# Optimization experiments

Hardware: AMD Instinct MI355X
Metric: run time of the kernel (lower is better)

The kernel has to match this reference:

```python
import jax, jax.numpy as jnp
import numpy as np

EPS = 1e-12  # F.normalize default eps


def _unfold(x, k, pad, stride):
    # torch F.unfold: [B,C,H,W] -> [B, C*k*k, L], features ordered (c, kh, kw), L row-major.
    B, C, H, W = x.shape
    xp = jnp.pad(x, ((0, 0), (0, 0), (pad, pad), (pad, pad)))
    Ho = (H + 2 * pad - k) // stride + 1
    Wo = (W + 2 * pad - k) // stride + 1
    r = (jnp.arange(Ho) * stride)[:, None] + jnp.arange(k)[None, :]  # [Ho,k]
    c = (jnp.arange(Wo) * stride)[:, None] + jnp.arange(k)[None, :]  # [Wo,k]
    p = xp[:, :, r[:, None, :, None], c[None, :, None, :]]  # [B,C,Ho,Wo,k,k]
    return p.transpose(0, 1, 4, 5, 2, 3).reshape(B, C * k * k, Ho * Wo)


def _fold(p, out_hw, k, pad, stride):
    # torch F.fold: overlap-add inverse of _unfold.
    B, CKK, L = p.shape
    C = CKK // (k * k)
    H, W = out_hw
    Ho = (H + 2 * pad - k) // stride + 1
    Wo = (W + 2 * pad - k) // stride + 1
    p = p.reshape(B, C, k, k, Ho, Wo).transpose(0, 1, 4, 5, 2, 3)  # [B,C,Ho,Wo,k,k]
    r = (jnp.arange(Ho) * stride)[:, None] + jnp.arange(k)[None, :]
    c = (jnp.arange(Wo) * stride)[:, None] + jnp.arange(k)[None, :]
    out = jnp.zeros((B, C, H + 2 * pad, W + 2 * pad), p.dtype)
    out = out.at[:, :, r[:, None, :, None], c[None, :, None, :]].add(p)
    return out[:, :, pad:pad + H, pad:pad + W]


def _l2n(x, axis):
    n = jnp.sqrt(jnp.sum(x * x, axis=axis, keepdims=True))
    return x / jnp.maximum(n, EPS)


def setup_inputs() -> dict:
    key = jax.random.key(0)
    ks = jax.random.split(key, 11)
    B, H, W = 1, 32, 32
    f = jnp.float32
    return {
        'lrsr_lv3': jax.random.normal(ks[0], (B, 256, H, W), f),
        'refsr_lv1': jax.random.normal(ks[1], (B, 64, 4 * H, 4 * W), f),
        'refsr_lv2': jax.random.normal(ks[2], (B, 128, 2 * H, 2 * W), f),
        'refsr_lv3': jax.random.normal(ks[3], (B, 256, H, W), f),
        'ref_lv1': jax.random.normal(ks[4], (B, 64, 4 * H, 4 * W), f),
        'ref_lv2': jax.random.normal(ks[5], (B, 128, 2 * H, 2 * W), f),
        'ref_lv3': jax.random.normal(ks[6], (B, 256, H, W), f),
        'W1': jax.random.normal(ks[7], (2304, 1152), f) * 0.02,
        'b1': jax.random.normal(ks[8], (2304,), f) * 0.02,
        'W2': jax.random.normal(ks[9], (2304, 576), f) * 0.02,
        'b2': jax.random.normal(ks[10], (2304,), f) * 0.02,
    }


def reference(lrsr_lv3, refsr_lv1, refsr_lv2, refsr_lv3, ref_lv1, ref_lv2, ref_lv3, W1, b1, W2, b2):
    B, _, H, W = lrsr_lv3.shape
    lr3 = _unfold(lrsr_lv3, 3, 1, 1)                       # [B, 2304, N]
    r3 = _unfold(refsr_lv3, 3, 1, 1).transpose(0, 2, 1)    # [B, N3, 2304]
    r2 = _unfold(refsr_lv2, 3, 1, 1).transpose(0, 2, 1) @ W1.T + b1  # [B, N2, 2304]
    r1 = _unfold(refsr_lv1, 3, 1, 1).transpose(0, 2, 1) @ W2.T + b2  # [B, N1, 2304]
    r3 = _l2n(r3, 2); r2 = _l2n(r2, 2); r1 = _l2n(r1, 2)
    lr3 = _l2n(lr3, 1)
    R3 = jnp.einsum('bnd,bdm->bnm', r3, lr3)  # [B, N3, N]
    R2 = jnp.einsum('bnd,bdm->bnm', r2, lr3)  # [B, N2, N]
    R1 = jnp.einsum('bnd,bdm->bnm', r1, lr3)  # [B, N1, N]
    R3_star = jnp.max(R3, axis=1); R3_arg = jnp.argmax(R3, axis=1)
    R2_star = jnp.max(R2, axis=1)
    R1_star = jnp.max(R1, axis=1)
    ref3u = _unfold(ref_lv3, 3, 1, 1)
    ref2u = _unfold(ref_lv2, 6, 2, 2)
    ref1u = _unfold(ref_lv1, 12, 4, 4)
    idx = R3_arg[:, None, :]  # [B,1,N] broadcast over feature dim
    T3u = jnp.take_along_axis(ref3u, idx, axis=2)
    T2u = jnp.take_along_axis(ref2u, idx, axis=2)
    T1u = jnp.take_along_axis(ref1u, idx, axis=2)
    T_lv3 = _fold(T3u, (H, W), 3, 1, 1) / 9.0
    T_lv2 = _fold(T2u, (2 * H, 2 * W), 6, 2, 2) / 9.0
    T_lv1 = _fold(T1u, (4 * H, 4 * W), 12, 4, 4) / 9.0
    S_3 = R3_star.reshape(B, 1, H, W)
    S_2 = R2_star.reshape(B, 1, H, W)
    S_1 = R1_star.reshape(B, 1, H, W)
    return (S_1, S_2, S_3, T_lv3, T_lv2, T_lv1)
```

## Files before the change

### kernel.cpp

```cpp
#include <hip/hip_runtime.h>

typedef short bf8 __attribute__((ext_vector_type(8)));
typedef float f32x4 __attribute__((ext_vector_type(4)));

static __device__ __forceinline__ unsigned short f2bf(float f) {
  unsigned u = __float_as_uint(f);
  unsigned r = u + 0x7FFFu + ((u >> 16) & 1u);
  return (unsigned short)(r >> 16);
}
static __device__ __forceinline__ float bf2f(unsigned short h) {
  return __uint_as_float(((unsigned)h) << 16);
}
static __device__ __forceinline__ unsigned fkey(float f) {
  unsigned u = __float_as_uint(f);
  return (u & 0x80000000u) ? ~u : (u | 0x80000000u);
}
static __device__ __forceinline__ float kdec(unsigned k) {
  unsigned u = (k & 0x80000000u) ? (k & 0x7FFFFFFFu) : ~k;
  return __uint_as_float(u);
}
static __device__ __forceinline__ int xcdswz(int h, int nwg) {
  int q = nwg >> 3, r = nwg & 7;
  int xcd = h & 7, w = h >> 3;
  return (xcd < r ? xcd * (q + 1) : r * (q + 1) + (xcd - r) * q) + w;
}
static __device__ __forceinline__ int xcdbal(int h, int nwg, int nb0) {
  int xcd = h & 7, w = h >> 3;
  int qa = nb0 >> 3, qb = (nwg - nb0) >> 3;
  return (w < qa) ? (xcd * qa + w) : (nb0 + xcd * qb + (w - qa));
}
static __device__ __forceinline__ float win9s(const float* __restrict__ b, int m) {
  int mi = m >> 5, mj = m & 31;
  float s = 0.f;
#pragma unroll
  for (int dy = -1; dy <= 1; ++dy) {
    int i = mi + dy; if ((unsigned)i >= 32u) continue;
#pragma unroll
    for (int dx = -1; dx <= 1; ++dx) {
      int jx = mj + dx; if ((unsigned)jx >= 32u) continue;
      s += b[i * 32 + jx];
    }
  }
  return s;
}

static __device__ __forceinline__ void gload_lds16(const unsigned short* g, unsigned short* l) {
  __builtin_amdgcn_global_load_lds((const __attribute__((address_space(1))) void*)g,
                                   (__attribute__((address_space(3))) void*)l, 16, 0, 0);
}

static __device__ __forceinline__ float uf3(const float* __restrict__ src, int lgS, int d, int m) {
  const int S = 1 << lgS;
  int cc = d / 9;
  int r9 = d - cc * 9;
  int ki = r9 / 3;
  int kj = r9 - ki * 3;
  int i = (m >> lgS) + ki - 1;
  int j = (m & (S - 1)) + kj - 1;
  if ((unsigned)i >= (unsigned)S || (unsigned)j >= (unsigned)S) return 0.f;
  return src[((size_t)cc << (2 * lgS)) + ((size_t)i << lgS) + j];
}

__global__ __launch_bounds__(256) void k_prepA(const float* __restrict__ lrsr3, const float* __restrict__ rsr3,
                                               const float* __restrict__ rsr2, const float* __restrict__ rsr1,
                                               const float* __restrict__ W1, const float* __restrict__ W2,
                                               const float* __restrict__ b1, const float* __restrict__ b2,
                                               float* __restrict__ G2,
                                               float* __restrict__ rsr2t, float* __restrict__ rsr1t,
                                               unsigned short* __restrict__ lr3nbT,
                                               unsigned short* __restrict__ W1t, unsigned short* __restrict__ W2t,
                                               float* __restrict__ sclw, float* __restrict__ scu3w,
                                               float* __restrict__ D1, float* __restrict__ D2) {
  __shared__ __align__(16) unsigned char smem[18432];
  const int blk = blockIdx.x;
  const int tid = threadIdx.x;
  if (blk < 4) {
    float* b1L = (float*)smem;
    float* b2L = b1L + 2304;
    const int p = blk * 256 + tid;
    for (int i = tid; i < 2304; i += 256) { b1L[i] = b1[i]; b2L[i] = b2[i]; }
    __syncthreads();
    float d1a[9] = {}, d2a[9] = {};
    for (int cc = 0; cc < 256; ++cc) {
      float v = lrsr3[(size_t)cc * 1024 + p];
#pragma unroll
      for (int kk = 0; kk < 9; ++kk) {
        d1a[kk] = fmaf(b1L[cc * 9 + kk], v, d1a[kk]);
        d2a[kk] = fmaf(b2L[cc * 9 + kk], v, d2a[kk]);
      }
    }
#pragma unroll
    for (int kk = 0; kk < 9; ++kk) { D1[kk * 1024 + p] = d1a[kk]; D2[kk * 1024 + p] = d2a[kk]; }
  } else if (blk < 6) {
    float* ss = (float*)smem;
    const float* src = (blk == 4) ? lrsr3 : rsr3;
    float a4[4] = {0.f, 0.f, 0.f, 0.f};
    for (int cc = 0; cc < 256; ++cc) {
#pragma unroll
      for (int k = 0; k < 4; ++k) {
        float v = src[(size_t)cc * 1024 + k * 256 + tid];
        a4[k] = fmaf(v, v, a4[k]);
      }
    }
#pragma unroll
    for (int k = 0; k < 4; ++k) ss[k * 256 + tid] = a4[k];
    __syncthreads();
    float* dst = (blk == 4) ? sclw : scu3w;
#pragma unroll
    for (int k = 0; k < 4; ++k) {
      int m = k * 256 + tid;
      dst[m] = 1.f / fmaxf(sqrtf(win9s(ss, m)), 1e-12f);
    }
  } else if (blk < 1030) {
    float (*As)[32] = (float(*)[32])smem;
    float (*Bs)[32] = (float(*)[32])(smem + 2048);
    const int px = blk - 6;
    const int m0 = (px >> 5) * 32, n0 = (px & 31) * 32;
    const int tx = tid & 15, ty = tid >> 4;
    float acc[2][2] = {};
    for (int kb = 0; kb < 256; kb += 16) {
      __syncthreads();
      {
        int kk = tid >> 5, mm = tid & 31;
        As[kk][mm] = lrsr3[(size_t)(kb + kk) * 1024 + m0 + mm];
        Bs[kk][mm] = rsr3[(size_t)(kb + kk) * 1024 + n0 + mm];
        int e2 = tid + 256; int kk2 = e2 >> 5, mm2 = e2 & 31;
        As[kk2][mm2] = lrsr3[(size_t)(kb + kk2) * 1024 + m0 + mm2];
        Bs[kk2][mm2] = rsr3[(size_t)(kb + kk2) * 1024 + n0 + mm2];
      }
      __syncthreads();
#pragma unroll
      for (int kk = 0; kk < 16; ++kk) {
        float a0 = As[kk][ty * 2], a1 = As[kk][ty * 2 + 1];
        float b0 = Bs[kk][tx * 2], b1v = Bs[kk][tx * 2 + 1];
        acc[0][0] = fmaf(a0, b0, acc[0][0]); acc[0][1] = fmaf(a0, b1v, acc[0][1]);
        acc[1][0] = fmaf(a1, b0, acc[1][0]); acc[1][1] = fmaf(a1, b1v, acc[1][1]);
      }
    }
#pragma unroll
    for (int i = 0; i < 2; ++i)
#pragma unroll
      for (int jj = 0; jj < 2; ++jj)
        G2[(size_t)(m0 + ty * 2 + i) * 1024 + (n0 + tx * 2 + jj)] = acc[i][jj];
  } else if (blk < 1158) {
    float (*Tt)[65] = (float(*)[65])smem;
    const int idx = blk - 1030;
    const int ct = idx & 1, st = idx >> 1;
#pragma unroll
    for (int i = 0; i < 16; ++i) {
      int id = tid + i * 256;
      int r = id >> 6, c = id & 63;
      Tt[r][c] = rsr2[(size_t)(ct * 64 + r) * 4096 + st * 64 + c];
    }
    __syncthreads();
#pragma unroll
    for (int i = 0; i < 16; ++i) {
      int id = tid + i * 256;
      int cc2 = id >> 6, rr = id & 63;
      rsr2t[(size_t)(st * 64 + cc2) * 128 + ct * 64 + rr] = Tt[rr][cc2];
    }
  } else if (blk < 1414) {
    float (*Tt)[65] = (float(*)[65])smem;
    const int st = blk - 1158;
#pragma unroll
    for (int i = 0; i < 16; ++i) {
      int id = tid + i * 256;
      int r = id >> 6, c = id & 63;
      Tt[r][c] = rsr1[(size_t)r * 16384 + st * 64 + c];
    }
    __syncthreads();
#pragma unroll
    for (int i = 0; i < 16; ++i) {
      int id = tid + i * 256;
      int cc2 = id >> 6, rr = id & 63;
      rsr1t[(size_t)(st * 64 + cc2) * 64 + rr] = Tt[rr][cc2];
    }
  } else if (blk < 2566) {
    int id8 = (blk - 1414) * 256 + tid;
    int m = id8 / 288, c0 = (id8 - m * 288) * 8;
    bf8 v;
#pragma unroll
    for (int e = 0; e < 8; ++e) v[e] = (short)f2bf(uf3(lrsr3, 5, c0 + e, m));
    *(bf8*)(lr3nbT + (size_t)m * 2304 + c0) = v;
  } else {
    unsigned short (*Ls)[65] = (unsigned short(*)[65])smem;
    int idx = blk - 2566;
    int xx = idx % 27, yy = idx / 27;
    const float* W; unsigned short* Wt; int Cw, c0;
    if (xx < 18) { W = W1; Wt = W1t; Cw = 1152; c0 = xx * 64; }
    else         { W = W2; Wt = W2t; Cw = 576;  c0 = (xx - 18) * 64; }
    const int Cch = Cw / 9;
    const int d0 = yy * 64;
#pragma unroll
    for (int i = 0; i < 16; ++i) {
      int id = tid + i * 256;
      int r = id >> 6, c = id & 63;
      Ls[r][c] = f2bf(W[(size_t)(d0 + r) * Cw + c0 + c]);
    }
    __syncthreads();
#pragma unroll
    for (int i = 0; i < 16; ++i) {
      int id = tid + i * 256;
      int cc = id >> 6, rr = id & 63;
      int c = c0 + cc;
      Wt[(size_t)((c % 9) * Cch + c / 9) * 2304 + d0 + rr] = Ls[rr][cc];
    }
  }
}

struct Job {
  const unsigned short* Alo;
  const unsigned short* Ahi;
  const unsigned short* Bt;
  unsigned short* Clo;
  unsigned short* Chi;
  const float* bl;
  const float* bw;
  const float* bbp;
  const float* rowscale;
  float* pnsq;
  float* pbwd;
  float* cmax;
  int Msplit, N, K, nbx, Mtot, npart, which;
};

template <int EPI, int NBUF>
static __device__ __forceinline__ void gemm_body(const Job& j0, const Job& j1, int nb0, int bid) {
  __shared__ __align__(16) unsigned short As[NBUF][128 * 64];
  __shared__ __align__(16) unsigned short Bs[NBUF][128 * 64];
  __shared__ unsigned colkey[128];
  __shared__ float ninvL[128];

  const bool first = (bid < nb0);
  const Job j = first ? j0 : j1;
  const int local = bid - (first ? 0 : nb0);
  const int by = local / j.nbx;
  const int bx = local - by * j.nbx;
  const int m0 = by * 128, n0 = bx * 128;
  const int K = j.K, N = j.N;

  const unsigned short* Abase = (m0 < j.Msplit)
      ? j.Alo + (size_t)m0 * K
      : j.Ahi + (size_t)(m0 - j.Msplit) * K;

  const int tid = threadIdx.x;
  const int l = tid & 63;
  const int w = tid >> 6;
  const int wr = w >> 1, wc = w & 1;
  if (EPI == 2) {
    if (tid < 128) {
      colkey[tid] = 0u;
      const int r = m0 + tid;
      float nsq = 0.f, bwd = 0.f;
      for (int p = 0; p < j.npart; ++p) {
        nsq += j.pnsq[(size_t)p * j.Mtot + r];
        bwd += j.pbwd[(size_t)p * j.Mtot + r];
      }
      float tq = nsq + 2.f * bwd + j.bbp[j.which];
      ninvL[tid] = 1.f / fmaxf(sqrtf(fmaxf(tq, 0.f)), 1e-12f);
    }
  }

  f32x4 acc[4][4] = {};

  const int srow = w * 32;
  const int lrow = l >> 3;
  const int gcol = ((l & 7) ^ lrow) * 8;
  const int mr = l & 15;
  const int kg = l >> 4;

  const int nt = K >> 6;
  const int snap_kb = n0 + wc * 64;
  unsigned short snap[4][4][4];

  auto stage = [&](int buf, int kb) {
#pragma unroll
    for (int i = 0; i < 4; ++i) {
      int r = srow + i * 8;
      gload_lds16(Abase + (size_t)(r + lrow) * K + kb + gcol, &As[buf][r * 64]);
      gload_lds16(j.Bt + (size_t)(n0 + r + lrow) * K + kb + gcol, &Bs[buf][r * 64]);
    }
  };
  auto compute_tile = [&](int cur) {
#pragma unroll
    for (int ks = 0; ks < 2; ++ks) {
      bf8 af[4], bv[4];
#pragma unroll
      for (int mi = 0; mi < 4; ++mi) {
        const int row = wr * 64 + mi * 16 + mr;
        af[mi] = *(const bf8*)&As[cur][row * 64 + (((ks * 4 + kg) ^ (row & 7)) * 8)];
      }
#pragma unroll
      for (int ni = 0; ni < 4; ++ni) {
        const int row = wc * 64 + ni * 16 + mr;
        bv[ni] = *(const bf8*)&Bs[cur][row * 64 + (((ks * 4 + kg) ^ (row & 7)) * 8)];
      }
      __builtin_amdgcn_s_setprio(1);
#pragma unroll
      for (int mi = 0; mi < 4; ++mi)
#pragma unroll
        for (int ni = 0; ni < 4; ++ni)
          acc[mi][ni] = __builtin_amdgcn_mfma_f32_16x16x32_bf16(af[mi], bv[ni], acc[mi][ni], 0, 0, 0);
      __builtin_amdgcn_s_setprio(0);
    }
  };
  auto do_snap = [&](int cur) {
#pragma unroll
    for (int mi = 0; mi < 4; ++mi)
#pragma unroll
      for (int e = 0; e < 4; ++e) {
        const int row = wr * 64 + mi * 16 + kg * 4 + e;
#pragma unroll
        for (int ni = 0; ni < 4; ++ni) {
          const int slot = ni * 2 + (mr >> 3);
          snap[mi][ni][e] = As[cur][row * 64 + ((slot ^ (row & 7)) * 8) + (mr & 7)];
        }
      }
  };

  if constexpr (NBUF == 1) {
    for (int t = 0; t < nt; ++t) {
      if (t) __syncthreads();
      stage(0, t << 6);
      __syncthreads();
      compute_tile(0);
      if (EPI == 1 && (t << 6) == snap_kb) do_snap(0);
    }
  } else {
    auto waitv = [&](int Wt) {
      if (Wt >= 2)      asm volatile("s_waitcnt vmcnt(16)\ns_barrier" ::: "memory");
      else if (Wt == 1) asm volatile("s_waitcnt vmcnt(8)\ns_barrier" ::: "memory");
      else              asm volatile("s_waitcnt vmcnt(0)\ns_barrier" ::: "memory");
    };
#pragma unroll
    for (int p = 0; p < NBUF; ++p) if (p < nt) stage(p, p << 6);
    { int inflight = (NBUF < nt ? NBUF : nt); waitv(inflight - 1); }
    int cur = 0;
    for (int t = 0; t < nt; ++t) {
      compute_tile(cur);
      if (EPI == 1 && (t << 6) == snap_kb) do_snap(cur);
      if (t + 1 < nt) {
        asm volatile("s_waitcnt lgkmcnt(0)\ns_barrier" ::: "memory");
        if (t + NBUF < nt) stage(cur, (t + NBUF) << 6);
        const int im = (nt - 1 < t + NBUF) ? (nt - 1) : (t + NBUF);
        waitv(im - (t + 1));
        cur = (cur + 1 == NBUF) ? 0 : cur + 1;
      }
    }
  }

  const int lr0 = wr * 64;
  const int lc0 = wc * 64;
  if (EPI == 0) {
    const bool hi = (m0 >= j.Msplit);
    unsigned short* Cbase = hi ? j.Chi + (size_t)(m0 - j.Msplit) * N
                               : j.Clo + (size_t)m0 * N;
    float rs[4][4];
#pragma unroll
    for (int mi = 0; mi < 4; ++mi)
#pragma unroll
      for (int e = 0; e < 4; ++e)
        rs[mi][e] = hi ? j.rowscale[m0 - j.Msplit + lr0 + mi * 16 + kg * 4 + e] : 1.f;
#pragma unroll
    for (int mi = 0; mi < 4; ++mi)
#pragma unroll
      for (int ni = 0; ni < 4; ++ni)
#pragma unroll
        for (int e = 0; e < 4; ++e)
          Cbase[(size_t)(lr0 + mi * 16 + kg * 4 + e) * (size_t)N + (n0 + lc0 + ni * 16 + mr)] =
              f2bf(acc[mi][ni][e] * rs[mi][e]);
  } else if (EPI == 1) {
    float rp[4][4] = {};
    float bp[4][4] = {};
#pragma unroll
    for (int ni = 0; ni < 4; ++ni) {
      const float bwv = j.bw[n0 + lc0 + ni * 16 + mr];
#pragma unroll
      for (int mi = 0; mi < 4; ++mi)
#pragma unroll
        for (int e = 0; e < 4; ++e) {
          const float av = bf2f(snap[mi][ni][e]);
          rp[mi][e] += acc[mi][ni][e] * av;
          bp[mi][e] += bwv * av;
        }
    }
#pragma unroll
    for (int off = 1; off < 16; off <<= 1)
#pragma unroll
      for (int mi = 0; mi < 4; ++mi)
#pragma unroll
        for (int e = 0; e < 4; ++e) {
          rp[mi][e] += __shfl_xor(rp[mi][e], off);
          bp[mi][e] += __shfl_xor(bp[mi][e], off);
        }
    if (mr == 0) {
      const size_t slotbase = (size_t)(bx * 2 + wc) * j.Mtot;
#pragma unroll
      for (int mi = 0; mi < 4; ++mi)
#pragma unroll
        for (int e = 0; e < 4; ++e) {
          const int r = m0 + lr0 + mi * 16 + kg * 4 + e;
          j.pnsq[slotbase + r] = rp[mi][e];
          j.pbwd[slotbase + r] = bp[mi][e];
        }
    }
  } else {
    float nv[4][4];
#pragma unroll
    for (int mi = 0; mi < 4; ++mi)
#pragma unroll
      for (int e = 0; e < 4; ++e)
        nv[mi][e] = ninvL[lr0 + mi * 16 + kg * 4 + e];
#pragma unroll
    for (int ni = 0; ni < 4; ++ni) {
      float blv = j.bl[n0 + lc0 + ni * 16 + mr];
      float mx = -3.0e38f;
#pragma unroll
      for (int mi = 0; mi < 4; ++mi)
#pragma unroll
        for (int e = 0; e < 4; ++e) mx = fmaxf(mx, (acc[mi][ni][e] + blv) * nv[mi][e]);
      atomicMax(&colkey[lc0 + ni * 16 + mr], fkey(mx));
    }
    __syncthreads();
    if (tid < 128) j.cmax[(size_t)by * 1024 + n0 + tid] = kdec(colkey[tid]);
  }
}

__global__ __launch_bounds__(256) void k_prepBP(Job pa, Job pb, int nbP0,
                                                const float* __restrict__ rsr2t, const float* __restrict__ rsr1t,
                                                const float* __restrict__ W1, const float* __restrict__ W2,
                                                const float* __restrict__ b1, const float* __restrict__ b2,
                                                const float* __restrict__ sclw, const float* __restrict__ scu3w,
                                                const float* __restrict__ D1, const float* __restrict__ D2,
                                                const float* __restrict__ G2,
                                                unsigned short* __restrict__ U2b, unsigned short* __restrict__ U1b,
                                                float* __restrict__ bw2, float* __restrict__ bw1,
                                                float* __restrict__ bb,
                                                float* __restrict__ bl2, float* __restrict__ bl1,
                                                float* __restrict__ s3, int* __restrict__ arg) {
  const int blk = blockIdx.x;
  const int tid = threadIdx.x;
  if (blk < 218) {
    gemm_body<0, 1>(pa, pb, nbP0, xcdswz(blk, 218));
  } else if (blk < 2522) {
    int id = (blk - 218) * 256 + tid;
    int t = id & 15, rest = id >> 4;
    int kk = rest % 9, n = rest / 9;
    int cc0 = t * 8;
    int ki = kk / 3, kj = kk - ki * 3;
    int sy = (n >> 6) + ki - 1, sx = (n & 63) + kj - 1;
    bf8 v;
    if ((unsigned)sy < 64u && (unsigned)sx < 64u) {
      const float* p = rsr2t + (size_t)(sy * 64 + sx) * 128 + cc0;
      f32x4 a = *(const f32x4*)p;
      f32x4 bq = *(const f32x4*)(p + 4);
#pragma unroll
      for (int e = 0; e < 4; ++e) { v[e] = (short)f2bf(a[e]); v[4 + e] = (short)f2bf(bq[e]); }
    } else {
#pragma unroll
      for (int e = 0; e < 8; ++e) v[e] = 0;
    }
    *(bf8*)(U2b + (size_t)n * 1152 + kk * 128 + cc0) = v;
  } else if (blk < 7642) {
    int id = (blk - 2522) * 256 + tid;
    int n = id / 80, rem = id - n * 80;
    int ks = rem >> 3, t = rem & 7;
    int cc0 = t * 8;
    bf8 v;
    if (ks == 9) {
#pragma unroll
      for (int e = 0; e < 8; ++e) v[e] = 0;
    } else {
      int ki = ks / 3, kj = ks - ki * 3;
      int sy = (n >> 7) + ki - 1, sx = (n & 127) + kj - 1;
      if ((unsigned)sy < 128u && (unsigned)sx < 128u) {
        const float* p = rsr1t + (size_t)(sy * 128 + sx) * 64 + cc0;
        f32x4 a = *(const f32x4*)p;
        f32x4 bq = *(const f32x4*)(p + 4);
#pragma unroll
        for (int e = 0; e < 4; ++e) { v[e] = (short)f2bf(a[e]); v[4 + e] = (short)f2bf(bq[e]); }
      } else {
#pragma unroll
        for (int e = 0; e < 8; ++e) v[e] = 0;
      }
    }
    *(bf8*)(U1b + (size_t)n * 640 + ks * 64 + cc0) = v;
  } else if (blk < 7722) {
    __shared__ float red[256];
    int idx = blk - 7642;
    int x = idx & 7, y = idx >> 3;
    if (y == 9) {
      if (x >= 2) return;
      const float* b = x ? b2 : b1;
      float s = 0.f;
      for (int d = tid; d < 2304; d += 256) s += b[d] * b[d];
      red[tid] = s; __syncthreads();
      for (int o = 128; o > 0; o >>= 1) { if (tid < o) red[tid] += red[tid + o]; __syncthreads(); }
      if (tid == 0) bb[x] = red[0];
      return;
    }
    const bool two = x < 5;
    const float* W = two ? W1 : W2;
    const float* b = two ? b1 : b2;
    float* bw = two ? bw2 : bw1;
    const int Cw = two ? 1152 : 576;
    int c = (two ? x : x - 5) * 256 + tid;
    if (c >= Cw) return;
    int d0 = y * 256;
    float s = 0.f;
    for (int d = d0; d < d0 + 256; ++d) s += b[d] * W[(size_t)d * Cw + c];
    atomicAdd(&bw[(c % 9) * (Cw / 9) + c / 9], s);
  } else if (blk < 8746) {
    __shared__ float bv[256]; __shared__ int bidx[256];
    const int m = blk - 7722;
    const int mi = m >> 5, mj = m & 31;
    float best = -3.0e38f; int bi = 0;
    for (int n = tid; n < 1024; n += 256) {
      const int ni = n >> 5, nj = n & 31;
      float raw = 0.f;
#pragma unroll
      for (int dy = -1; dy <= 1; ++dy) {
#pragma unroll
        for (int dx = -1; dx <= 1; ++dx) {
          bool vm = ((unsigned)(mi + dy) < 32u) && ((unsigned)(mj + dx) < 32u);
          bool vn = ((unsigned)(ni + dy) < 32u) && ((unsigned)(nj + dx) < 32u);
          if (vm && vn) {
            int off = dy * 32 + dx;
            raw += G2[(size_t)(m + off) * 1024 + (n + off)];
          }
        }
      }
      float v = raw * scu3w[n];
      if (v > best) { best = v; bi = n; }
    }
    bv[tid] = best; bidx[tid] = bi;
    __syncthreads();
    for (int o = 128; o > 0; o >>= 1) {
      if (tid < o) {
        float ov = bv[tid + o]; int oi = bidx[tid + o];
        if (ov > bv[tid] || (ov == bv[tid] && oi < bidx[tid])) { bv[tid] = ov; bidx[tid] = oi; }
      }
      __syncthreads();
    }
    if (tid == 0) { s3[m] = bv[0] * sclw[m]; arg[m] = bidx[0]; }
  } else {
    int m = (blk - 8746) * 256 + tid;
    int mi = m >> 5, mj = m & 31;
    float a1 = 0.f, a2 = 0.f;
#pragma unroll
    for (int ki = 0; ki < 3; ++ki) {
      int i = mi + ki - 1; if ((unsigned)i >= 32u) continue;
#pragma unroll
      for (int kj = 0; kj < 3; ++kj) {
        int jx = mj + kj - 1; if ((unsigned)jx >= 32u) continue;
        int pix = i * 32 + jx;
        int kk = ki * 3 + kj;
        a1 += D1[kk * 1024 + pix];
        a2 += D2[kk * 1024 + pix];
      }
    }
    float sc = sclw[m];
    bl2[m] = a1 * sc;
    bl1[m] = a2 * sc;
  }
}

__global__ __launch_bounds__(256) void k_gE1(Job a, Job b, int nb0) {
  gemm_body<1, 1>(a, b, nb0, xcdbal((int)blockIdx.x, (int)gridDim.x, nb0));
}
__global__ __launch_bounds__(256) void k_gE2(Job a, Job b, int nb0) {
  gemm_body<2, 1>(a, b, nb0, xcdbal((int)blockIdx.x, (int)gridDim.x, nb0));
}

__global__ __launch_bounds__(256) void k_tfold(const float* __restrict__ ref3, const float* __restrict__ ref2,
                                               const float* __restrict__ ref1, const int* __restrict__ arg,
                                               const float* __restrict__ cmax1, const float* __restrict__ cmax2,
                                               float* __restrict__ out) {
  const int bid = blockIdx.x;
  const int tid = threadIdx.x;
  if (bid < 256) {
    __shared__ float plane[1024];
    __shared__ int argL[1024];
    const int c = bid;
#pragma unroll
    for (int k = 0; k < 4; ++k) {
      plane[k * 256 + tid] = ref3[(size_t)c * 1024 + k * 256 + tid];
      argL[k * 256 + tid] = arg[k * 256 + tid];
    }
    __syncthreads();
#pragma unroll
    for (int k = 0; k < 4; ++k) {
      int px = k * 256 + tid;
      int y = px >> 5, x = px & 31;
      float s = 0.f;
#pragma unroll
      for (int di = -1; di <= 1; ++di) {
        int i = y + di;
        if ((unsigned)i >= 32u) continue;
#pragma unroll
        for (int dj = -1; dj <= 1; ++dj) {
          int jw = x + dj;
          if ((unsigned)jw >= 32u) continue;
          int n2 = argL[i * 32 + jw];
          int rr = (n2 >> 5) + y - i, cc = (n2 & 31) + x - jw;
          if ((unsigned)rr < 32u && (unsigned)cc < 32u) s += plane[rr * 32 + cc];
        }
      }
      out[3072 + (size_t)c * 1024 + px] = s * (1.f / 9.f);
    }
  } else if (bid < 1280) {
    __shared__ int argL[1024];
#pragma unroll
    for (int k = 0; k < 4; ++k) argL[k * 256 + tid] = arg[k * 256 + tid];
    __syncthreads();
    int id2 = (bid - 256) * 256 + tid;
    int q = id2 & 31, y = (id2 >> 5) & 63, c = id2 >> 11;
    int iy = y >> 1;
    float s0 = 0.f, s1 = 0.f;
#pragma unroll
    for (int di = -1; di <= 1; ++di) {
      int i = iy + di;
      if ((unsigned)i >= 32u) continue;
      int ry = y - 2 * i;
#pragma unroll
      for (int dj = -1; dj <= 1; ++dj) {
        int jw = q + dj;
        if ((unsigned)jw >= 32u) continue;
        int n2 = argL[i * 32 + jw];
        int rr = (n2 >> 5) * 2 + ry;
        int cb = (n2 & 31) * 2 + 2 * (q - jw);
        if ((unsigned)rr < 64u && (unsigned)cb < 63u) {
          const float* p = ref2 + (size_t)c * 4096 + rr * 64 + cb;
          s0 += p[0]; s1 += p[1];
        }
      }
    }
    float2 o; o.x = s0 * (1.f / 9.f); o.y = s1 * (1.f / 9.f);
    *(float2*)(out + 265216 + (size_t)c * 4096 + y * 64 + 2 * q) = o;
  } else if (bid < 2304) {
    __shared__ int argL[1024];
#pragma unroll
    for (int k = 0; k < 4; ++k) argL[k * 256 + tid] = arg[k * 256 + tid];
    __syncthreads();
    int id1 = (bid - 1280) * 256 + tid;
    int q = id1 & 31, y = (id1 >> 5) & 127, c = id1 >> 12;
    int iy = y >> 2;
    f32x4 s = {0.f, 0.f, 0.f, 0.f};
#pragma unroll
    for (int di = -1; di <= 1; ++di) {
      int i = iy + di;
      if ((unsigned)i >= 32u) continue;
      int ry = y - 4 * i;
#pragma unroll
      for (int dj = -1; dj <= 1; ++dj) {
        int jw = q + dj;
        if ((unsigned)jw >= 32u) continue;
        int n2 = argL[i * 32 + jw];
        int rr = (n2 >> 5) * 4 + ry;
        int cb = (n2 & 31) * 4 + 4 * (q - jw);
        if ((unsigned)rr < 128u && (unsigned)cb < 125u) {
          f32x4 v = *(const f32x4*)(ref1 + (size_t)c * 16384 + rr * 128 + cb);
          s += v;
        }
      }
    }
    s *= (1.f / 9.f);
    *(f32x4*)(out + 789504 + (size_t)c * 16384 + y * 128 + 4 * q) = s;
  } else {
    int t = (bid - 2304) * 256 + tid;
    if (t < 1024) {
      float mx = -3.0e38f;
      for (int rb = 0; rb < 128; ++rb) mx = fmaxf(mx, cmax1[rb * 1024 + t]);
      out[t] = mx;
    } else {
      int tt = t - 1024;
      float mx = -3.0e38f;
      for (int rb = 0; rb < 32; ++rb) mx = fmaxf(mx, cmax2[rb * 1024 + tt]);
      out[1024 + tt] = mx;
    }
  }
}

static constexpr size_t OFF_BW2     = 0;
static constexpr size_t OFF_BW1     = 4608;
static constexpr size_t ZERO_BYTES  = 7168;
static constexpr size_t OFF_BB      = 7168;
static constexpr size_t OFF_BL2     = 7424;
static constexpr size_t OFF_BL1     = 11520;
static constexpr size_t OFF_SCLW    = 15616;
static constexpr size_t OFF_SCU3W   = 19712;
static constexpr size_t OFF_R3ARG   = 23808;
static constexpr size_t OFF_PNSQ2   = 27904;
static constexpr size_t OFF_PBWD2   = OFF_PNSQ2 + 294912;
static constexpr size_t OFF_PNSQ1   = OFF_PBWD2 + 294912;
static constexpr size_t OFF_PBWD1   = OFF_PNSQ1 + 655360;
static constexpr size_t OFF_CMAX2   = OFF_PBWD1 + 655360;
static constexpr size_t OFF_CMAX1   = OFF_CMAX2 + 131072;
static constexpr size_t OFF_LR3NBT  = OFF_CMAX1 + 524288;
static constexpr size_t OFF_U2B     = OFF_LR3NBT + 4718592;
static constexpr size_t OFF_U1B     = OFF_U2B    + 9437184;
static constexpr size_t OFF_W1T     = OFF_U1B    + 20971520;
static constexpr size_t OFF_W2T     = OFF_W1T    + 5308416;
static constexpr size_t OFF_A2      = OFF_W2T    + 2949120;
static constexpr size_t OFF_A1      = OFF_A2     + 2654208;
static constexpr size_t OFF_M2T     = OFF_A1     + 819200;
static constexpr size_t OFF_M1T     = OFF_M2T    + 2359296;
static constexpr size_t OFF_G2      = OFF_M1T    + 1310720;
static constexpr size_t OFF_R2T     = OFF_G2     + 4194304;
static constexpr size_t OFF_R1T     = OFF_R2T    + 2097152;
static constexpr size_t OFF_D1      = OFF_R1T    + 4194304;
static constexpr size_t OFF_D2      = OFF_D1     + 36864;

extern "C" void kernel_launch(void* const* d_in, const int* in_sizes, int n_in,
                              void* d_out, int out_size, void* d_ws, size_t ws_size,
                              hipStream_t stream) {
  (void)in_sizes; (void)n_in; (void)out_size; (void)ws_size;
  const float* lrsr3  = (const float*)d_in[0];
  const float* rsr1   = (const float*)d_in[1];
  const float* rsr2   = (const float*)d_in[2];
  const float* rsr3   = (const float*)d_in[3];
  const float* ref1   = (const float*)d_in[4];
  const float* ref2   = (const float*)d_in[5];
  const float* ref3   = (const float*)d_in[6];
  const float* W1     = (const float*)d_in[7];
  const float* b1     = (const float*)d_in[8];
  const float* W2     = (const float*)d_in[9];
  const float* b2     = (const float*)d_in[10];
  float* out = (float*)d_out;
  char* ws = (char*)d_ws;

  float*          bw2     = (float*)(ws + OFF_BW2);
  float*          bw1     = (float*)(ws + OFF_BW1);
  float*          bb      = (float*)(ws + OFF_BB);
  float*          bl2     = (float*)(ws + OFF_BL2);
  float*          bl1     = (float*)(ws + OFF_BL1);
  float*          sclw    = (float*)(ws + OFF_SCLW);
  float*          scu3w   = (float*)(ws + OFF_SCU3W);
  int*            R3arg   = (int*)(ws + OFF_R3ARG);
  float*          pnsq2   = (float*)(ws + OFF_PNSQ2);
  float*          pbwd2   = (float*)(ws + OFF_PBWD2);
  float*          pnsq1   = (float*)(ws + OFF_PNSQ1);
  float*          pbwd1   = (float*)(ws + OFF_PBWD1);
  float*          cmax2   = (float*)(ws + OFF_CMAX2);
  float*          cmax1   = (float*)(ws + OFF_CMAX1);
  unsigned short* lr3nbT  = (unsigned short*)(ws + OFF_LR3NBT);
  unsigned short* U2b     = (unsigned short*)(ws + OFF_U2B);
  unsigned short* U1b     = (unsigned short*)(ws + OFF_U1B);
  unsigned short* W1t     = (unsigned short*)(ws + OFF_W1T);
  unsigned short* W2t     = (unsigned short*)(ws + OFF_W2T);
  unsigned short* A2b     = (unsigned short*)(ws + OFF_A2);
  unsigned short* A1b     = (unsigned short*)(ws + OFF_A1);
  unsigned short* M2tb    = (unsigned short*)(ws + OFF_M2T);
  unsigned short* M1tb    = (unsigned short*)(ws + OFF_M1T);
  float*          G2      = (float*)(ws + OFF_G2);
  float*          rsr2t   = (float*)(ws + OFF_R2T);
  float*          rsr1t   = (float*)(ws + OFF_R1T);
  float*          D1      = (float*)(ws + OFF_D1);
  float*          D2      = (float*)(ws + OFF_D2);

  hipMemsetAsync(d_ws, 0, ZERO_BYTES, stream);
  hipMemsetAsync(ws + OFF_W2T + (size_t)576 * 2304 * 2, 0, (size_t)64 * 2304 * 2, stream);

  k_prepA<<<3538, 256, 0, stream>>>(lrsr3, rsr3, rsr2, rsr1, W1, W2, b1, b2,
                                    G2, rsr2t, rsr1t, lr3nbT, W1t, W2t, sclw, scu3w, D1, D2);

  Job jz = {};
  {
    Job a = jz, b = jz;
    a.Alo = W1t; a.Ahi = lr3nbT; a.Msplit = 1152; a.Bt = W1t;
    a.Clo = A2b; a.Chi = M2tb; a.rowscale = sclw; a.N = 1152; a.K = 2304; a.nbx = 9;
    b.Alo = W2t; b.Ahi = lr3nbT; b.Msplit = 640; b.Bt = W2t;
    b.Clo = A1b; b.Chi = M1tb; b.rowscale = sclw; b.N = 640; b.K = 2304; b.nbx = 5;
    k_prepBP<<<8750, 256, 0, stream>>>(a, b, 153, rsr2t, rsr1t, W1, W2, b1, b2,
                                       sclw, scu3w, D1, D2, G2,
                                       U2b, U1b, bw2, bw1, bb, bl2, bl1, out + 2048, R3arg);
  }
  {
    Job a = jz, b = jz;
    a.Alo = U2b; a.Ahi = U2b; a.Msplit = 4096; a.Bt = A2b;
    a.bw = bw2; a.pnsq = pnsq2; a.pbwd = pbwd2; a.Mtot = 4096;
    a.N = 1152; a.K = 1152; a.nbx = 9;
    b.Alo = U1b; b.Ahi = U1b; b.Msplit = 16384; b.Bt = A1b;
    b.bw = bw1; b.pnsq = pnsq1; b.pbwd = pbwd1; b.Mtot = 16384;
    b.N = 640; b.K = 640; b.nbx = 5;
    k_gE1<<<288 + 640, 256, 0, stream>>>(a, b, 288);
  }
  {
    Job a = jz, b = jz;
    a.Alo = U2b; a.Ahi = U2b; a.Msplit = 4096; a.Bt = M2tb;
    a.bl = bl2; a.pnsq = pnsq2; a.pbwd = pbwd2; a.bbp = bb;
    a.npart = 18; a.which = 0; a.cmax = cmax2; a.Mtot = 4096;
    a.N = 1024; a.K = 1152; a.nbx = 8;
    b.Alo = U1b; b.Ahi = U1b; b.Msplit = 16384; b.Bt = M1tb;
    b.bl = bl1; b.pnsq = pnsq1; b.pbwd = pbwd1; b.bbp = bb;
    b.npart = 10; b.which = 1; b.cmax = cmax1; b.Mtot = 16384;
    b.N = 1024; b.K = 640; b.nbx = 8;
    k_gE2<<<256 + 1024, 256, 0, stream>>>(a, b, 256);
  }

  k_tfold<<<2312, 256, 0, stream>>>(ref3, ref2, ref1, R3arg, cmax1, cmax2, out);
}
```

Measured before the change: 208.4 us.

## Fuse texture fold gather into first GEMM launch, split final max-reduce

Moves the T_lv3/T_lv2/T_lv1 fold-gather work (which depends only on R3 argmax from the prep kernel) into the same launch as the first epilogue GEMM, so it runs concurrently instead of after the second GEMM. The remaining column-max reduction gets its own small kernel. Shared memory becomes a single byte buffer carved per branch. This adds launch width to the GEMM kernel and may raise its shared-memory footprint or register pressure, reducing occupancy.

```diff
diff --git a/kernel.cpp b/kernel.cpp
--- a/kernel.cpp
+++ b/kernel.cpp
@@ -225,11 +225,12 @@
 };
 
 template <int EPI, int NBUF>
-static __device__ __forceinline__ void gemm_body(const Job& j0, const Job& j1, int nb0, int bid) {
-  __shared__ __align__(16) unsigned short As[NBUF][128 * 64];
-  __shared__ __align__(16) unsigned short Bs[NBUF][128 * 64];
-  __shared__ unsigned colkey[128];
-  __shared__ float ninvL[128];
+static __device__ __forceinline__ void gemm_body(const Job& j0, const Job& j1, int nb0, int bid,
+                                                 unsigned char* smem) {
+  unsigned short (*As)[128 * 64] = (unsigned short(*)[128 * 64])smem;
+  unsigned short (*Bs)[128 * 64] = (unsigned short(*)[128 * 64])(smem + (size_t)NBUF * 16384);
+  unsigned* colkey = (unsigned*)(smem + (size_t)2 * NBUF * 16384);
+  float* ninvL = (float*)(smem + (size_t)2 * NBUF * 16384 + 512);
 
   const bool first = (bid < nb0);
   const Job j = first ? j0 : j1;
@@ -438,10 +439,11 @@
                                                 float* __restrict__ bb,
                                                 float* __restrict__ bl2, float* __restrict__ bl1,
                                                 float* __restrict__ s3, int* __restrict__ arg) {
+  __shared__ __align__(16) unsigned char sm[33792];
   const int blk = blockIdx.x;
   const int tid = threadIdx.x;
   if (blk < 218) {
-    gemm_body<0, 1>(pa, pb, nbP0, xcdswz(blk, 218));
+    gemm_body<0, 1>(pa, pb, nbP0, xcdswz(blk, 218), sm);
   } else if (blk < 2522) {
     int id = (blk - 218) * 256 + tid;
     int t = id & 15, rest = id >> 4;
@@ -486,7 +488,7 @@
     }
     *(bf8*)(U1b + (size_t)n * 640 + ks * 64 + cc0) = v;
   } else if (blk < 7722) {
-    __shared__ float red[256];
+    float* red = (float*)sm;
     int idx = blk - 7642;
     int x = idx & 7, y = idx >> 3;
     if (y == 9) {
@@ -511,7 +513,8 @@
     for (int d = d0; d < d0 + 256; ++d) s += b[d] * W[(size_t)d * Cw + c];
     atomicAdd(&bw[(c % 9) * (Cw / 9) + c / 9], s);
   } else if (blk < 8746) {
-    __shared__ float bv[256]; __shared__ int bidx[256];
+    float* bv = (float*)sm;
+    int* bidx = (int*)(sm + 1024);
     const int m = blk - 7722;
     const int mi = m >> 5, mj = m & 31;
     float best = -3.0e38f; int bi = 0;
@@ -565,23 +568,19 @@
   }
 }
 
-__global__ __launch_bounds__(256) void k_gE1(Job a, Job b, int nb0) {
-  gemm_body<1, 1>(a, b, nb0, xcdbal((int)blockIdx.x, (int)gridDim.x, nb0));
-}
-__global__ __launch_bounds__(256) void k_gE2(Job a, Job b, int nb0) {
-  gemm_body<2, 1>(a, b, nb0, xcdbal((int)blockIdx.x, (int)gridDim.x, nb0));
-}
-
-__global__ __launch_bounds__(256) void k_tfold(const float* __restrict__ ref3, const float* __restrict__ ref2,
-                                               const float* __restrict__ ref1, const int* __restrict__ arg,
-                                               const float* __restrict__ cmax1, const float* __restrict__ cmax2,
-                                               float* __restrict__ out) {
+__global__ __launch_bounds__(256) void k_gE1F(Job a, Job b, int nb0,
+                                              const float* __restrict__ ref3, const float* __restrict__ ref2,
+                                              const float* __restrict__ ref1, const int* __restrict__ arg,
+                                              float* __restrict__ out) {
+  __shared__ __align__(16) unsigned char sm[33792];
   const int bid = blockIdx.x;
   const int tid = threadIdx.x;
-  if (bid < 256) {
-    __shared__ float plane[1024];
-    __shared__ int argL[1024];
-    const int c = bid;
+  if (bid < 928) {
+    gemm_body<1, 1>(a, b, nb0, xcdbal(bid, 928, nb0), sm);
+  } else if (bid < 1184) {
+    float* plane = (float*)sm;
+    int* argL = (int*)(sm + 4096);
+    const int c = bid - 928;
 #pragma unroll
     for (int k = 0; k < 4; ++k) {
       plane[k * 256 + tid] = ref3[(size_t)c * 1024 + k * 256 + tid];
@@ -608,12 +607,12 @@
       }
       out[3072 + (size_t)c * 1024 + px] = s * (1.f / 9.f);
     }
-  } else if (bid < 1280) {
-    __shared__ int argL[1024];
+  } else if (bid < 2208) {
+    int* argL = (int*)sm;
 #pragma unroll
     for (int k = 0; k < 4; ++k) argL[k * 256 + tid] = arg[k * 256 + tid];
     __syncthreads();
-    int id2 = (bid - 256) * 256 + tid;
+    int id2 = (bid - 1184) * 256 + tid;
     int q = id2 & 31, y = (id2 >> 5) & 63, c = id2 >> 11;
     int iy = y >> 1;
     float s0 = 0.f, s1 = 0.f;
@@ -637,12 +636,12 @@
     }
     float2 o; o.x = s0 * (1.f / 9.f); o.y = s1 * (1.f / 9.f);
     *(float2*)(out + 265216 + (size_t)c * 4096 + y * 64 + 2 * q) = o;
-  } else if (bid < 2304) {
-    __shared__ int argL[1024];
+  } else {
+    int* argL = (int*)sm;
 #pragma unroll
     for (int k = 0; k < 4; ++k) argL[k * 256 + tid] = arg[k * 256 + tid];
     __syncthreads();
-    int id1 = (bid - 1280) * 256 + tid;
+    int id1 = (bid - 2208) * 256 + tid;
     int q = id1 & 31, y = (id1 >> 5) & 127, c = id1 >> 12;
     int iy = y >> 2;
     f32x4 s = {0.f, 0.f, 0.f, 0.f};
@@ -666,18 +665,26 @@
     }
     s *= (1.f / 9.f);
     *(f32x4*)(out + 789504 + (size_t)c * 16384 + y * 128 + 4 * q) = s;
+  }
+}
+
+__global__ __launch_bounds__(256) void k_gE2(Job a, Job b, int nb0) {
+  __shared__ __align__(16) unsigned char sm[33792];
+  gemm_body<2, 1>(a, b, nb0, xcdbal((int)blockIdx.x, (int)gridDim.x, nb0), sm);
+}
+
+__global__ __launch_bounds__(256) void k_sfin(const float* __restrict__ cmax1, const float* __restrict__ cmax2,
+                                              float* __restrict__ out) {
+  int t = blockIdx.x * 256 + threadIdx.x;
+  if (t < 1024) {
+    float mx = -3.0e38f;
+    for (int rb = 0; rb < 128; ++rb) mx = fmaxf(mx, cmax1[rb * 1024 + t]);
+    out[t] = mx;
   } else {
-    int t = (bid - 2304) * 256 + tid;
-    if (t < 1024) {
-      float mx = -3.0e38f;
-      for (int rb = 0; rb < 128; ++rb) mx = fmaxf(mx, cmax1[rb * 1024 + t]);
-      out[t] = mx;
-    } else {
-      int tt = t - 1024;
-      float mx = -3.0e38f;
-      for (int rb = 0; rb < 32; ++rb) mx = fmaxf(mx, cmax2[rb * 1024 + tt]);
-      out[1024 + tt] = mx;
-    }
+    int tt = t - 1024;
+    float mx = -3.0e38f;
+    for (int rb = 0; rb < 32; ++rb) mx = fmaxf(mx, cmax2[rb * 1024 + tt]);
+    out[1024 + tt] = mx;
   }
 }
 
@@ -783,7 +790,7 @@
     b.Alo = U1b; b.Ahi = U1b; b.Msplit = 16384; b.Bt = A1b;
     b.bw = bw1; b.pnsq = pnsq1; b.pbwd = pbwd1; b.Mtot = 16384;
     b.N = 640; b.K = 640; b.nbx = 5;
-    k_gE1<<<288 + 640, 256, 0, stream>>>(a, b, 288);
+    k_gE1F<<<3232, 256, 0, stream>>>(a, b, 288, ref3, ref2, ref1, R3arg, out);
   }
   {
     Job a = jz, b = jz;
@@ -798,5 +805,5 @@
     k_gE2<<<256 + 1024, 256, 0, stream>>>(a, b, 256);
   }
 
-  k_tfold<<<2312, 256, 0, stream>>>(ref3, ref2, ref1, R3arg, cmax1, cmax2, out);
-}
+  k_sfin<<<8, 256, 0, stream>>>(cmax1, cmax2, out);
+}
```

Measured after the change: 208.9 us. No clear change (+0.2%).
